# Optimization experiments

Measured on AMD Instinct MI355X. Metric: run time of the kernel, lower is better.

The kernel has to match this reference:

```python
import jax, jax.numpy as jnp
import numpy as np

K = 3  # kernel size
PAD = 1
C_IN = 32
C_OUT = 32
CKK = C_IN * K * K  # 288
HID = C_OUT  # hidden width of kernel-generator MLP


def _unfold(x):
    """torch F.unfold equivalent, (C, kh, kw)-major. x: [B,C,H,W] -> [B, C*K*K, H*W]."""
    B, C, H, W = x.shape
    xp = jnp.pad(x, ((0, 0), (0, 0), (PAD, PAD), (PAD, PAD)))
    # stack K*K shifted views -> [B, C, K*K, H, W]
    patches = jnp.stack(
        [xp[:, :, i:i + H, j:j + W] for i in range(K) for j in range(K)], axis=2
    )
    return patches.reshape(B, C * K * K, H * W)


def setup_inputs() -> dict:
    key = jax.random.key(0)
    ks = jax.random.split(key, 6)
    B, H, W = 2, 64, 64
    x = jax.random.normal(ks[0], (B, C_IN, H, W), dtype=jnp.float32)
    # kernel_generator: Linear(CKK -> HID), Tanh, Linear(HID -> C_OUT*CKK)
    s1 = 1.0 / np.sqrt(CKK)
    s2 = 1.0 / np.sqrt(HID)
    W1 = jax.random.uniform(ks[1], (HID, CKK), jnp.float32, -s1, s1)
    b1 = jax.random.uniform(ks[2], (HID,), jnp.float32, -s1, s1)
    W2 = jax.random.uniform(ks[3], (C_OUT * CKK, HID), jnp.float32, -s2, s2)
    b2 = jax.random.uniform(ks[4], (C_OUT * CKK,), jnp.float32, -s2, s2)
    bias = jax.random.uniform(ks[5], (C_OUT,), jnp.float32, -s1, s1)
    return {"x": x, "W1": W1, "b1": b1, "W2": W2, "b2": b2, "bias": bias}


def reference(x, W1, b1, W2, b2, bias):
    B, C, H, W = x.shape
    L = H * W
    u = _unfold(x)                       # [B, CKK, L]
    ut = u.transpose(0, 2, 1)            # [B, L, CKK]
    h = jnp.tanh(jnp.einsum('blj,hj->blh', ut, W1) + b1)          # [B, L, HID]
    kern = jnp.einsum('blh,oh->blo', h, W2) + b2                  # [B, L, C_OUT*CKK]
    kern = kern.reshape(B, L, C_OUT, CKK)                         # per-pixel kernels
    out = jnp.einsum('bloj,blj->bol', kern, ut)                   # [B, C_OUT, L]
    out = out.reshape(B, C_OUT, H, W) + bias[None, :, None, None]
    return out
```

## Files before the change

kernel.cpp:

```cpp
#include <hip/hip_runtime.h>
#include <hip/hip_bf16.h>


#define CKK 288
#define SJ  296

typedef __attribute__((ext_vector_type(8))) short short8;
typedef __attribute__((ext_vector_type(4))) float f32x4;

#define W2F_OFF 0
#define W1B_OFF 294912
#define B2B_OFF (294912 + 9216)
#define WS_ELEMS (294912 + 9216 + 9216)

__global__ __launch_bounds__(256) void prep_kernel(
    const float* __restrict__ W1, const float* __restrict__ W2,
    const float* __restrict__ b2, __hip_bfloat16* __restrict__ ws)
{
    int idx = blockIdx.x * 256 + threadIdx.x;
    if (idx < 294912) {
        int e  = idx & 7;
        int l  = (idx >> 3) & 63;
        int ck = idx >> 9;
        int w8 = ck / 9, kb = ck - w8 * 9;
        int o  = w8 >> 1;
        int h  = (w8 & 1) * 16 + (l & 15);
        int j  = kb * 32 + ((l >> 4) << 3) + e;
        ws[W2F_OFF + idx] = __float2bfloat16(W2[(o * CKK + j) * 32 + h]);
    } else if (idx < 294912 + 9216) {
        int k = idx - 294912;
        ws[W1B_OFF + k] = __float2bfloat16(W1[k]);
    } else if (idx < WS_ELEMS) {
        int k = idx - (294912 + 9216);
        ws[B2B_OFF + k] = __float2bfloat16(b2[k]);
    }
}

__global__ __launch_bounds__(512) void dynaconv_main(
    const float* __restrict__ x,
    const float* __restrict__ b1,
    const float* __restrict__ bias,
    const __hip_bfloat16* __restrict__ ws,
    float* __restrict__ out)
{
    __shared__ __hip_bfloat16 u_lds[32 * SJ];
    __shared__ float hh_lds[32 * 33];
    __shared__ float o_lds[32 * 33];

    const int t  = threadIdx.x;
    const int w  = t >> 6;
    const int l  = t & 63;
    const int lg = l >> 4;
    const int lr = l & 15;

    const int g0  = blockIdx.x * 32;
    const int b   = g0 >> 12;
    const int l0  = g0 & 4095;
    const int y   = l0 >> 6;
    const int wx0 = l0 & 63;

    #pragma unroll
    for (int k = 0; k < 18; ++k) {
        int idx = k * 512 + t;
        int j = idx >> 5, p = idx & 31;
        int c = j / 9, r = j - c * 9;
        int ki = r / 3, kj = r - ki * 3;
        int y2 = y + ki - 1;
        int x2 = wx0 + p + kj - 1;
        float v = 0.f;
        if ((unsigned)y2 < 64u && (unsigned)x2 < 64u)
            v = x[((b * 32 + c) * 64 + y2) * 64 + x2];
        u_lds[p * SJ + j] = __float2bfloat16(v);
    }
    __syncthreads();

    if (w < 4) {
        const __hip_bfloat16* Bmat = ws + ((w < 2) ? B2B_OFF : W1B_OFF);
        const int col = ((w & 1) * 16) + lr;
        f32x4 acc0 = {0.f, 0.f, 0.f, 0.f}, acc1 = {0.f, 0.f, 0.f, 0.f};
        #pragma unroll
        for (int kb = 0; kb < 9; ++kb) {
            short8 bf = *(const short8*)(Bmat + col * CKK + kb * 32 + lg * 8);
            short8 a0 = *(const short8*)(u_lds + lr * SJ + kb * 32 + lg * 8);
            short8 a1 = *(const short8*)(u_lds + (16 + lr) * SJ + kb * 32 + lg * 8);
            acc0 = __builtin_amdgcn_mfma_f32_16x16x32_bf16(a0, bf, acc0, 0, 0, 0);
            acc1 = __builtin_amdgcn_mfma_f32_16x16x32_bf16(a1, bf, acc1, 0, 0, 0);
        }
        if (w < 2) {
            float bv = bias[col];
            #pragma unroll
            for (int r = 0; r < 4; ++r) {
                o_lds[(lg * 4 + r) * 33 + col]        = acc0[r] + bv;
                o_lds[(16 + lg * 4 + r) * 33 + col]   = acc1[r] + bv;
            }
        } else {
            float b1v = b1[col];
            #pragma unroll
            for (int r = 0; r < 4; ++r) {
                hh_lds[(lg * 4 + r) * 33 + col]       = tanhf(acc0[r] + b1v);
                hh_lds[(16 + lg * 4 + r) * 33 + col]  = tanhf(acc1[r] + b1v);
            }
        }
    }
    __syncthreads();

    f32x4 acc[2][8];
    #pragma unroll
    for (int m = 0; m < 2; ++m)
        #pragma unroll
        for (int nf = 0; nf < 8; ++nf)
            acc[m][nf] = f32x4{0.f, 0.f, 0.f, 0.f};

    {
        const __hip_bfloat16* W2f = ws + W2F_OFF;
        short8 bcur[8];
        #pragma unroll
        for (int nf = 0; nf < 8; ++nf)
            bcur[nf] = *(const short8*)(W2f + (size_t)((w * 8 + nf) * 9 + 0) * 512 + l * 8);

        #pragma unroll
        for (int kb = 0; kb < 9; ++kb) {
            short8 a0 = *(const short8*)(u_lds + lr * SJ + kb * 32 + lg * 8);
            short8 a1 = *(const short8*)(u_lds + (16 + lr) * SJ + kb * 32 + lg * 8);
            short8 bnext[8];
            if (kb < 8) {
                #pragma unroll
                for (int nf = 0; nf < 8; ++nf)
                    bnext[nf] = *(const short8*)(W2f + (size_t)((w * 8 + nf) * 9 + kb + 1) * 512 + l * 8);
            }
            #pragma unroll
            for (int nf = 0; nf < 8; ++nf) {
                acc[0][nf] = __builtin_amdgcn_mfma_f32_16x16x32_bf16(a0, bcur[nf], acc[0][nf], 0, 0, 0);
                acc[1][nf] = __builtin_amdgcn_mfma_f32_16x16x32_bf16(a1, bcur[nf], acc[1][nf], 0, 0, 0);
            }
            if (kb < 8) {
                #pragma unroll
                for (int nf = 0; nf < 8; ++nf)
                    bcur[nf] = bnext[nf];
            }
        }
    }

    #pragma unroll
    for (int ol = 0; ol < 4; ++ol) {
        const int o = w * 4 + ol;
        #pragma unroll
        for (int m = 0; m < 2; ++m) {
            #pragma unroll
            for (int r = 0; r < 4; ++r) {
                const int p = m * 16 + lg * 4 + r;
                float v = hh_lds[p * 33 + lr]      * acc[m][ol * 2][r]
                        + hh_lds[p * 33 + 16 + lr] * acc[m][ol * 2 + 1][r];
                v += __shfl_xor(v, 1);
                v += __shfl_xor(v, 2);
                v += __shfl_xor(v, 4);
                v += __shfl_xor(v, 8);
                if (lr == 0) o_lds[p * 33 + o] += v;
            }
        }
    }
    __syncthreads();

    #pragma unroll
    for (int k = 0; k < 2; ++k) {
        int idx = k * 512 + t;
        int o = idx >> 5, p = idx & 31;
        out[((size_t)(b * 32 + o)) * 4096 + l0 + p] = o_lds[p * 33 + o];
    }
}

extern "C" void kernel_launch(void* const* d_in, const int* in_sizes, int n_in,
                              void* d_out, int out_size, void* d_ws, size_t ws_size,
                              hipStream_t stream) {
    const float* x    = (const float*)d_in[0];
    const float* W1   = (const float*)d_in[1];
    const float* b1   = (const float*)d_in[2];
    const float* W2   = (const float*)d_in[3];
    const float* b2   = (const float*)d_in[4];
    const float* bias = (const float*)d_in[5];
    float* out = (float*)d_out;
    __hip_bfloat16* ws = (__hip_bfloat16*)d_ws;

    prep_kernel<<<(WS_ELEMS + 255) / 256, 256, 0, stream>>>(W1, W2, b2, ws);
    dynaconv_main<<<256, 512, 0, stream>>>(x, b1, bias, ws, out);
}
```

Measured before the change: 35.54 us.

## Split output channels across four blocks and coalesce W2 prep reads

The main kernel now launches 1024 blocks of 256 threads, each handling 32 pixels and 8 output channels, in place of 256 blocks covering all 32 channels. The goal is better occupancy and a smaller W2 slice per block. In exchange, each block redoes the unfold gather and the hidden-layer MFMA, so that work is repeated four times. The prep kernel now reads W2 coalesced and scatters the writes into the fragment layout, instead of gathering strided reads.

```diff
diff --git a/kernel.cpp b/kernel.cpp
--- a/kernel.cpp
+++ b/kernel.cpp
@@ -17,26 +17,25 @@
     const float* __restrict__ W1, const float* __restrict__ W2,
     const float* __restrict__ b2, __hip_bfloat16* __restrict__ ws)
 {
-    int idx = blockIdx.x * 256 + threadIdx.x;
-    if (idx < 294912) {
-        int e  = idx & 7;
-        int l  = (idx >> 3) & 63;
-        int ck = idx >> 9;
-        int w8 = ck / 9, kb = ck - w8 * 9;
-        int o  = w8 >> 1;
-        int h  = (w8 & 1) * 16 + (l & 15);
-        int j  = kb * 32 + ((l >> 4) << 3) + e;
-        ws[W2F_OFF + idx] = __float2bfloat16(W2[(o * CKK + j) * 32 + h]);
-    } else if (idx < 294912 + 9216) {
-        int k = idx - 294912;
+    int s = blockIdx.x * 256 + threadIdx.x;
+    if (s < 294912) {
+        int o = s / 9216, rem = s - o * 9216;
+        int j = rem >> 5, h = rem & 31;
+        int w8 = o * 2 + (h >> 4);
+        int kb = j >> 5;
+        int l  = ((j >> 3) & 3) * 16 + (h & 15);
+        int e  = j & 7;
+        ws[W2F_OFF + (w8 * 9 + kb) * 512 + l * 8 + e] = __float2bfloat16(W2[s]);
+    } else if (s < 294912 + 9216) {
+        int k = s - 294912;
         ws[W1B_OFF + k] = __float2bfloat16(W1[k]);
-    } else if (idx < WS_ELEMS) {
-        int k = idx - (294912 + 9216);
+    } else if (s < WS_ELEMS) {
+        int k = s - (294912 + 9216);
         ws[B2B_OFF + k] = __float2bfloat16(b2[k]);
     }
 }
 
-__global__ __launch_bounds__(512) void dynaconv_main(
+__global__ __launch_bounds__(256, 4) void dynaconv_main(
     const float* __restrict__ x,
     const float* __restrict__ b1,
     const float* __restrict__ bias,
@@ -45,7 +44,8 @@
 {
     __shared__ __hip_bfloat16 u_lds[32 * SJ];
     __shared__ float hh_lds[32 * 33];
-    __shared__ float o_lds[32 * 33];
+    __shared__ float t_lds[32 * 8];
+    __shared__ float o_stage[8][32];
 
     const int t  = threadIdx.x;
     const int w  = t >> 6;
@@ -53,15 +53,17 @@
     const int lg = l >> 4;
     const int lr = l & 15;
 
-    const int g0  = blockIdx.x * 32;
-    const int b   = g0 >> 12;
-    const int l0  = g0 & 4095;
-    const int y   = l0 >> 6;
+    const int nt = blockIdx.x & 3, mt = blockIdx.x >> 2;
+    const int o0 = nt * 8;
+    const int g0 = mt * 32;
+    const int b  = g0 >> 12;
+    const int l0 = g0 & 4095;
+    const int y  = l0 >> 6;
     const int wx0 = l0 & 63;
 
     #pragma unroll
-    for (int k = 0; k < 18; ++k) {
-        int idx = k * 512 + t;
+    for (int k = 0; k < 36; ++k) {
+        int idx = k * 256 + t;
         int j = idx >> 5, p = idx & 31;
         int c = j / 9, r = j - c * 9;
         int ki = r / 3, kj = r - ki * 3;
@@ -74,76 +76,84 @@
     }
     __syncthreads();
 
-    if (w < 4) {
-        const __hip_bfloat16* Bmat = ws + ((w < 2) ? B2B_OFF : W1B_OFF);
-        const int col = ((w & 1) * 16) + lr;
-        f32x4 acc0 = {0.f, 0.f, 0.f, 0.f}, acc1 = {0.f, 0.f, 0.f, 0.f};
+    if (w < 3) {
+        const __hip_bfloat16* w1b = ws + W1B_OFF;
+        const __hip_bfloat16* b2b = ws + B2B_OFF;
+        f32x4 acc0 = {0.f,0.f,0.f,0.f}, acc1 = {0.f,0.f,0.f,0.f};
         #pragma unroll
         for (int kb = 0; kb < 9; ++kb) {
-            short8 bf = *(const short8*)(Bmat + col * CKK + kb * 32 + lg * 8);
+            short8 bf;
+            if (w < 2)
+                bf = *(const short8*)(w1b + (w * 16 + lr) * CKK + kb * 32 + lg * 8);
+            else if (lr < 8)
+                bf = *(const short8*)(b2b + (o0 + lr) * CKK + kb * 32 + lg * 8);
+            else
+                bf = short8{0,0,0,0,0,0,0,0};
             short8 a0 = *(const short8*)(u_lds + lr * SJ + kb * 32 + lg * 8);
             short8 a1 = *(const short8*)(u_lds + (16 + lr) * SJ + kb * 32 + lg * 8);
             acc0 = __builtin_amdgcn_mfma_f32_16x16x32_bf16(a0, bf, acc0, 0, 0, 0);
             acc1 = __builtin_amdgcn_mfma_f32_16x16x32_bf16(a1, bf, acc1, 0, 0, 0);
         }
         if (w < 2) {
-            float bv = bias[col];
-            #pragma unroll
-            for (int r = 0; r < 4; ++r) {
-                o_lds[(lg * 4 + r) * 33 + col]        = acc0[r] + bv;
-                o_lds[(16 + lg * 4 + r) * 33 + col]   = acc1[r] + bv;
-            }
-        } else {
+            const int col = w * 16 + lr;
             float b1v = b1[col];
             #pragma unroll
             for (int r = 0; r < 4; ++r) {
-                hh_lds[(lg * 4 + r) * 33 + col]       = tanhf(acc0[r] + b1v);
-                hh_lds[(16 + lg * 4 + r) * 33 + col]  = tanhf(acc1[r] + b1v);
+                hh_lds[(lg * 4 + r) * 33 + col]      = tanhf(acc0[r] + b1v);
+                hh_lds[(16 + lg * 4 + r) * 33 + col] = tanhf(acc1[r] + b1v);
+            }
+        } else if (lr < 8) {
+            float bv = bias[o0 + lr];
+            #pragma unroll
+            for (int r = 0; r < 4; ++r) {
+                t_lds[(lg * 4 + r) * 8 + lr]      = acc0[r] + bv;
+                t_lds[(16 + lg * 4 + r) * 8 + lr] = acc1[r] + bv;
             }
         }
     }
     __syncthreads();
 
-    f32x4 acc[2][8];
+    f32x4 acc[2][4];
     #pragma unroll
     for (int m = 0; m < 2; ++m)
         #pragma unroll
-        for (int nf = 0; nf < 8; ++nf)
+        for (int nf = 0; nf < 4; ++nf)
             acc[m][nf] = f32x4{0.f, 0.f, 0.f, 0.f};
 
     {
         const __hip_bfloat16* W2f = ws + W2F_OFF;
-        short8 bcur[8];
+        const int ckbase = (o0 * 2 + w * 4) * 9;
+        short8 bcur[4];
         #pragma unroll
-        for (int nf = 0; nf < 8; ++nf)
-            bcur[nf] = *(const short8*)(W2f + (size_t)((w * 8 + nf) * 9 + 0) * 512 + l * 8);
+        for (int nf = 0; nf < 4; ++nf)
+            bcur[nf] = *(const short8*)(W2f + (size_t)(ckbase + nf * 9) * 512 + l * 8);
 
         #pragma unroll
         for (int kb = 0; kb < 9; ++kb) {
             short8 a0 = *(const short8*)(u_lds + lr * SJ + kb * 32 + lg * 8);
             short8 a1 = *(const short8*)(u_lds + (16 + lr) * SJ + kb * 32 + lg * 8);
-            short8 bnext[8];
+            short8 bnext[4];
             if (kb < 8) {
                 #pragma unroll
-                for (int nf = 0; nf < 8; ++nf)
-                    bnext[nf] = *(const short8*)(W2f + (size_t)((w * 8 + nf) * 9 + kb + 1) * 512 + l * 8);
+                for (int nf = 0; nf < 4; ++nf)
+                    bnext[nf] = *(const short8*)(W2f + (size_t)(ckbase + nf * 9 + kb + 1) * 512 + l * 8);
             }
             #pragma unroll
-            for (int nf = 0; nf < 8; ++nf) {
+            for (int nf = 0; nf < 4; ++nf) {
                 acc[0][nf] = __builtin_amdgcn_mfma_f32_16x16x32_bf16(a0, bcur[nf], acc[0][nf], 0, 0, 0);
                 acc[1][nf] = __builtin_amdgcn_mfma_f32_16x16x32_bf16(a1, bcur[nf], acc[1][nf], 0, 0, 0);
             }
             if (kb < 8) {
                 #pragma unroll
-                for (int nf = 0; nf < 8; ++nf)
+                for (int nf = 0; nf < 4; ++nf)
                     bcur[nf] = bnext[nf];
             }
         }
     }
 
     #pragma unroll
-    for (int ol = 0; ol < 4; ++ol) {
-        const int o = w * 4 + ol;
+    for (int ol = 0; ol < 2; ++ol) {
+        const int o_loc = w * 2 + ol;
         #pragma unroll
         for (int m = 0; m < 2; ++m) {
             #pragma unroll
@@ -155,17 +165,16 @@
                 v += __shfl_xor(v, 2);
                 v += __shfl_xor(v, 4);
                 v += __shfl_xor(v, 8);
-                if (lr == 0) o_lds[p * 33 + o] += v;
+                if (lr == 0) o_stage[o_loc][p] = v;
             }
         }
     }
     __syncthreads();
 
-    #pragma unroll
-    for (int k = 0; k < 2; ++k) {
-        int idx = k * 512 + t;
-        int o = idx >> 5, p = idx & 31;
-        out[((size_t)(b * 32 + o)) * 4096 + l0 + p] = o_lds[p * 33 + o];
+    {
+        int o_l = t >> 5, p = t & 31;
+        float val = o_stage[o_l][p] + t_lds[p * 8 + o_l];
+        out[((size_t)(b * 32 + o0 + o_l)) * 4096 + l0 + p] = val;
     }
 }
 
@@ -182,5 +191,5 @@
     __hip_bfloat16* ws = (__hip_bfloat16*)d_ws;
 
     prep_kernel<<<(WS_ELEMS + 255) / 256, 256, 0, stream>>>(W1, W2, b2, ws);
-    dynaconv_main<<<256, 512, 0, stream>>>(x, b1, bias, ws, out);
+    dynaconv_main<<<1024, 256, 0, stream>>>(x, b1, bias, ws, out);
 }
```

New measurement: 30.93 us. 1.15x faster.
